# Kernel tuning notes

Measured on AMD Instinct MI355X. Metric: run time of the kernel, lower is better.

## Reference

```python
import jax, jax.numpy as jnp
import numpy as np

B, P, C = 64, 8732, 81
NEG_POS_RATIO = 3


def _smooth_l1_masked_sum(p, t, maskf):
    # smooth_l1 with beta=1, sum reduction, restricted to positive priors
    d = jnp.abs(p - t)
    l = jnp.where(d < 1.0, 0.5 * d * d, d - 0.5)  # [B,P,K]
    return jnp.sum(l.sum(-1) * maskf)


def setup_inputs() -> dict:
    key = jax.random.key(0)
    ks = jax.random.split(key, 6)
    loc_data = jax.random.normal(ks[0], (B, P, 4), jnp.float32)
    conf_data = jax.random.normal(ks[1], (B, P, C), jnp.float32)
    four_corners_data = jax.random.normal(ks[2], (B, P, 8), jnp.float32)
    loc_t = jax.random.normal(ks[3], (B, P, 4), jnp.float32)
    four_corners_t = jax.random.normal(ks[4], (B, P, 8), jnp.float32)
    conf_t = jax.random.randint(ks[5], (B, P), 0, C, jnp.int32)
    return {
        "loc_data": loc_data,
        "conf_data": conf_data,
        "four_corners_data": four_corners_data,
        "loc_t": loc_t,
        "four_corners_t": four_corners_t,
        "conf_t": conf_t,
    }


def reference(loc_data, conf_data, four_corners_data, loc_t, four_corners_t, conf_t):
    num_priors = conf_data.shape[1]
    pos = conf_t > 0                                  # [B,P]
    posf = pos.astype(conf_data.dtype)

    # localization + four-corner smooth-L1 over matched (positive) priors
    loss_l = _smooth_l1_masked_sum(loc_data, loc_t, posf)
    loss_four_corners = _smooth_l1_masked_sum(four_corners_data, four_corners_t, posf)

    # per-prior CE loss: log_sum_exp(conf) - conf[target]
    lse = jax.nn.logsumexp(conf_data, axis=-1)        # [B,P]
    gathered = jnp.take_along_axis(conf_data, conf_t[..., None], axis=-1)[..., 0]
    ce_all = lse - gathered                           # [B,P]

    # hard-negative mining: rank negatives by CE loss (double argsort)
    loss_c_mine = jnp.where(pos, 0.0, ce_all)
    loss_idx = jnp.argsort(-loss_c_mine, axis=1)      # descending sort indices
    idx_rank = jnp.argsort(loss_idx, axis=1)          # rank of each prior
    num_pos = pos.sum(axis=1, keepdims=True)          # [B,1]
    num_neg = jnp.minimum(NEG_POS_RATIO * num_pos, num_priors - 1)
    neg = idx_rank < num_neg                          # [B,P]

    sel = pos | neg
    loss_c = jnp.sum(jnp.where(sel, ce_all, 0.0))

    N = num_pos.sum().astype(conf_data.dtype)
    return (loss_l / N, loss_c / N, loss_four_corners / N)
```

## Files before the change

kernel.cpp:

```cpp
#include <hip/hip_runtime.h>


#define NB 64
#define NP 8732
#define NC 81
constexpr int BP = NB * NP;
constexpr int PBLK = (NP + 255) / 256;

__device__ inline float sl1(float d) {
    d = fabsf(d);
    return d < 1.0f ? 0.5f * d * d : d - 0.5f;
}

__global__ void k_init(float* acc_area) {
    if (threadIdx.x < 194) acc_area[threadIdx.x] = 0.0f;
}

__global__ __launch_bounds__(256) void k_main(
    const float* __restrict__ loc_data, const float* __restrict__ conf_data,
    const float* __restrict__ fc_data,  const float* __restrict__ loc_t,
    const float* __restrict__ fc_t,     const int* __restrict__ conf_t,
    float* __restrict__ ce, float* __restrict__ acc,
    int* __restrict__ npos_b, float* __restrict__ spos_b, float* __restrict__ sneg_b)
{
    const int b  = blockIdx.y;
    const int t  = threadIdx.x;
    const int p0 = blockIdx.x << 8;
    const int nrows = min(256, NP - p0);

    __shared__ __align__(16) float tile[64 * NC + 4];
    __shared__ int   tgt_s[256];
    __shared__ float red[4][5];

    float l_sum = 0.0f, f_sum = 0.0f, sp = 0.0f, sn = 0.0f;
    int np = 0;

    {
        const int p = p0 + t;
        int tgt = 0;
        if (p < NP) {
            const size_t g = (size_t)b * NP + p;
            tgt = conf_t[g];
            const float posf = (tgt > 0) ? 1.0f : 0.0f;
            np = (tgt > 0) ? 1 : 0;
            float4 a4  = ((const float4*)loc_data)[g];
            float4 a4t = ((const float4*)loc_t)[g];
            l_sum = (sl1(a4.x - a4t.x) + sl1(a4.y - a4t.y) +
                     sl1(a4.z - a4t.z) + sl1(a4.w - a4t.w)) * posf;
            float4 c0 = ((const float4*)fc_data)[2 * g];
            float4 c1 = ((const float4*)fc_data)[2 * g + 1];
            float4 d0 = ((const float4*)fc_t)[2 * g];
            float4 d1 = ((const float4*)fc_t)[2 * g + 1];
            f_sum = (sl1(c0.x - d0.x) + sl1(c0.y - d0.y) + sl1(c0.z - d0.z) + sl1(c0.w - d0.w) +
                     sl1(c1.x - d1.x) + sl1(c1.y - d1.y) + sl1(c1.z - d1.z) + sl1(c1.w - d1.w)) * posf;
        }
        tgt_s[t] = tgt;
    }

    const size_t gbase = ((size_t)b * NP + p0) * (size_t)NC;
    const int al = (int)(gbase & 3);
    const float* conf_al = conf_data + (gbase - (size_t)al);
    const int r = t >> 2, sub = t & 3;

    for (int s = 0; s < 4; ++s) {
        const int r0 = s << 6;
        const int rs = min(64, nrows - r0);
        if (rs <= 0) break;
        const int nf  = al + rs * NC;
        const int n4  = nf >> 2;
        const int rem = nf & 3;

        __syncthreads();
        const float4* src4 = (const float4*)(conf_al + (size_t)r0 * NC);
        float4* dst4 = (float4*)tile;
        for (int j = t; j < n4; j += 256) dst4[j] = src4[j];
        if (t < rem) tile[(n4 << 2) + t] = conf_al[(size_t)r0 * NC + (n4 << 2) + t];
        __syncthreads();

        if (r < rs) {
            const float* lrow = tile + al + r * NC;
            float s0 = 0.0f, s1 = 0.0f;
            int c = sub;
            #pragma unroll
            for (int k = 0; k < 10; ++k) {
                s0 += __expf(lrow[c]); c += 4;
                s1 += __expf(lrow[c]); c += 4;
            }
            if (sub == 0) s0 += __expf(lrow[80]);
            float ss = s0 + s1;
            ss += __shfl_xor(ss, 1, 64);
            ss += __shfl_xor(ss, 2, 64);
            if (sub == 0) {
                const int tgt = tgt_s[r0 + r];
                const float cev = __logf(ss) - lrow[tgt];
                ce[(size_t)b * NP + (size_t)(p0 + r0 + r)] = cev;
                if (tgt > 0) sp += cev; else sn += cev;
            }
        }
    }

    const int wave = t >> 6, lane = t & 63;
    float vnp = (float)np;
    #pragma unroll
    for (int o = 32; o; o >>= 1) {
        l_sum += __shfl_xor(l_sum, o, 64);
        f_sum += __shfl_xor(f_sum, o, 64);
        sp    += __shfl_xor(sp, o, 64);
        sn    += __shfl_xor(sn, o, 64);
        vnp   += __shfl_xor(vnp, o, 64);
    }
    if (lane == 0) {
        red[wave][0] = l_sum; red[wave][1] = f_sum;
        red[wave][2] = sp;    red[wave][3] = sn;   red[wave][4] = vnp;
    }
    __syncthreads();
    if (t == 0) {
        float rl = 0, rf = 0, rp = 0, rn = 0, rc = 0;
        #pragma unroll
        for (int w = 0; w < 4; ++w) {
            rl += red[w][0]; rf += red[w][1]; rp += red[w][2];
            rn += red[w][3]; rc += red[w][4];
        }
        atomicAdd(&acc[0], rl);
        atomicAdd(&acc[1], rf);
        atomicAdd(&spos_b[b], rp);
        atomicAdd(&sneg_b[b], rn);
        atomicAdd(&npos_b[b], (int)rc);
    }
}

__global__ __launch_bounds__(256) void k_batch(
    const float* __restrict__ ce, const int* __restrict__ conf_t,
    const int* __restrict__ npos_b, const float* __restrict__ spos_b,
    const float* __restrict__ sneg_b, float* __restrict__ loss_c_b)
{
    const int b = blockIdx.x;
    const int t = threadIdx.x;
    const int npos    = npos_b[b];
    const int nneg    = NP - npos;
    const int num_neg = min(3 * npos, NP - 1);

    if (num_neg >= nneg) {
        if (t == 0) loss_c_b[b] = spos_b[b] + sneg_b[b];
        return;
    }
    if (num_neg <= 0) {
        if (t == 0) loss_c_b[b] = spos_b[b];
        return;
    }

    __shared__ float ce_s[NP];
    __shared__ float sredf[4];
    __shared__ int   sredi[4];
    const float* crow = ce + (size_t)b * NP;
    const int*   trow = conf_t + (size_t)b * NP;
    for (int p = t; p < NP; p += 256)
        ce_s[p] = (trow[p] > 0) ? -1.0f : crow[p];
    __syncthreads();

    const int wave = t >> 6, lane = t & 63;
    const int K = num_neg;
    unsigned lo = 0u, hi = 0x7f800000u;
    while (lo < hi) {
        unsigned mid = lo + ((hi - lo) >> 1);
        float v = __uint_as_float(mid);
        int c_t = 0;
        for (int p = t; p < NP; p += 256) c_t += (ce_s[p] > v) ? 1 : 0;
        #pragma unroll
        for (int o = 32; o; o >>= 1) c_t += __shfl_xor(c_t, o, 64);
        __syncthreads();
        if (lane == 0) sredi[wave] = c_t;
        __syncthreads();
        int cnt = sredi[0] + sredi[1] + sredi[2] + sredi[3];
        if (cnt < K) hi = mid; else lo = mid + 1;
    }
    float v = __uint_as_float(lo);
    int c_t = 0; float s_t = 0.0f;
    for (int p = t; p < NP; p += 256) {
        float x = ce_s[p];
        if (x > v) { c_t++; s_t += x; }
    }
    #pragma unroll
    for (int o = 32; o; o >>= 1) {
        c_t += __shfl_xor(c_t, o, 64);
        s_t += __shfl_xor(s_t, o, 64);
    }
    __syncthreads();
    if (lane == 0) { sredi[wave] = c_t; sredf[wave] = s_t; }
    __syncthreads();
    if (t == 0) {
        int   cnt = sredi[0] + sredi[1] + sredi[2] + sredi[3];
        float sgt = sredf[0] + sredf[1] + sredf[2] + sredf[3];
        loss_c_b[b] = spos_b[b] + sgt + (float)(K - cnt) * v;
    }
}

__global__ void k_final(const float* __restrict__ acc,
                        const float* __restrict__ loss_c_b,
                        const int* __restrict__ npos_b,
                        float* __restrict__ out)
{
    const int t = threadIdx.x;
    float lc = loss_c_b[t];
    int   np = npos_b[t];
    #pragma unroll
    for (int o = 32; o; o >>= 1) {
        lc += __shfl_xor(lc, o, 64);
        np += __shfl_xor(np, o, 64);
    }
    if (t == 0) {
        float N = (float)np;
        out[0] = acc[0] / N;
        out[1] = lc / N;
        out[2] = acc[1] / N;
    }
}

extern "C" void kernel_launch(void* const* d_in, const int* in_sizes, int n_in,
                              void* d_out, int out_size, void* d_ws, size_t ws_size,
                              hipStream_t stream)
{
    const float* loc_data  = (const float*)d_in[0];
    const float* conf_data = (const float*)d_in[1];
    const float* fc_data   = (const float*)d_in[2];
    const float* loc_t     = (const float*)d_in[3];
    const float* fc_t      = (const float*)d_in[4];
    const int*   conf_t    = (const int*)d_in[5];
    float* out = (float*)d_out;

    float* ce       = (float*)d_ws;
    float* acc      = ce + BP;
    int*   npos_b   = (int*)(acc + 2);
    float* spos_b   = (float*)(npos_b + 64);
    float* sneg_b   = spos_b + 64;
    float* loss_c_b = sneg_b + 64;

    hipLaunchKernelGGL(k_init,  dim3(1), dim3(256), 0, stream, acc);
    hipLaunchKernelGGL(k_main,  dim3(PBLK, NB), dim3(256), 0, stream,
                       loc_data, conf_data, fc_data, loc_t, fc_t, conf_t,
                       ce, acc, npos_b, spos_b, sneg_b);
    hipLaunchKernelGGL(k_batch, dim3(NB), dim3(256), 0, stream,
                       ce, conf_t, npos_b, spos_b, sneg_b, loss_c_b);
    hipLaunchKernelGGL(k_final, dim3(1), dim3(64), 0, stream,
                       acc, loss_c_b, npos_b, out);
}
```

Before: 339.0 us.

## Double-buffer conf tiles with direct global-to-LDS loads in k_main

Replaces the synchronous float4 copy of 64-row conf tiles into shared memory with `global_load_lds` (16-byte) loads into two 32-row buffers. The next phase is prefetched while the current one is reduced, with manual `s_waitcnt` and barriers. Each row now uses 8 lanes instead of 4, with an extra shuffle step in the reduction. The goal is to overlap conf_data memory latency with the exp/log compute. The trade-offs are hand-written wait counts, extra barriers, and fixed 256-float chunk loads that can read slightly past the end of the final tile.

```diff
diff --git a/kernel.cpp b/kernel.cpp
--- a/kernel.cpp
+++ b/kernel.cpp
@@ -6,10 +6,19 @@
 #define NC 81
 constexpr int BP = NB * NP;
 constexpr int PBLK = (NP + 255) / 256;
+constexpr int PROWS = 32;
+constexpr int TFLOAT = 11 * 256;
 
 __device__ inline float sl1(float d) {
     d = fabsf(d);
     return d < 1.0f ? 0.5f * d * d : d - 0.5f;
+}
+
+__device__ __forceinline__ void gload_lds16(const float* g, float* l) {
+    __builtin_amdgcn_global_load_lds(
+        (const __attribute__((address_space(1))) void*)g,
+        (__attribute__((address_space(3))) void*)l,
+        16, 0, 0);
 }
 
 __global__ void k_init(float* acc_area) {
@@ -27,8 +36,9 @@
     const int t  = threadIdx.x;
     const int p0 = blockIdx.x << 8;
     const int nrows = min(256, NP - p0);
-
-    __shared__ __align__(16) float tile[64 * NC + 4];
+    const int nph   = (nrows + PROWS - 1) / PROWS;
+
+    __shared__ __align__(16) float tile[2][TFLOAT];
     __shared__ int   tgt_s[256];
     __shared__ float red[4][5];
 
@@ -60,46 +70,57 @@
     const size_t gbase = ((size_t)b * NP + p0) * (size_t)NC;
     const int al = (int)(gbase & 3);
     const float* conf_al = conf_data + (gbase - (size_t)al);
-    const int r = t >> 2, sub = t & 3;
-
-    for (int s = 0; s < 4; ++s) {
-        const int r0 = s << 6;
-        const int rs = min(64, nrows - r0);
-        if (rs <= 0) break;
-        const int nf  = al + rs * NC;
-        const int n4  = nf >> 2;
-        const int rem = nf & 3;
-
-        __syncthreads();
-        const float4* src4 = (const float4*)(conf_al + (size_t)r0 * NC);
-        float4* dst4 = (float4*)tile;
-        for (int j = t; j < n4; j += 256) dst4[j] = src4[j];
-        if (t < rem) tile[(n4 << 2) + t] = conf_al[(size_t)r0 * NC + (n4 << 2) + t];
-        __syncthreads();
-
+    const int wave = t >> 6, lane = t & 63;
+    const int r = t >> 3, sub = t & 7;
+
+    auto stage = [&](int s) {
+        const int rs  = min(PROWS, nrows - s * PROWS);
+        const int nch = (al + rs * NC + 255) >> 8;
+        const float* gb = conf_al + (size_t)s * (PROWS * NC);
+        float* lb = tile[s & 1];
+        #pragma unroll
+        for (int i = 0; i < 3; ++i) {
+            int c = wave + 4 * i;
+            c = c < nch ? c : nch - 1;
+            gload_lds16(gb + ((size_t)c << 8) + (lane << 2), lb + (c << 8));
+        }
+    };
+
+    stage(0);
+    for (int s = 0; s < nph; ++s) {
+        if (s + 1 < nph) {
+            stage(s + 1);
+            asm volatile("s_waitcnt vmcnt(3)\n\ts_barrier" ::: "memory");
+        } else {
+            asm volatile("s_waitcnt vmcnt(0)\n\ts_barrier" ::: "memory");
+        }
+
+        const int rs = min(PROWS, nrows - s * PROWS);
         if (r < rs) {
-            const float* lrow = tile + al + r * NC;
+            const float* lrow = tile[s & 1] + al + r * NC;
             float s0 = 0.0f, s1 = 0.0f;
             int c = sub;
             #pragma unroll
-            for (int k = 0; k < 10; ++k) {
-                s0 += __expf(lrow[c]); c += 4;
-                s1 += __expf(lrow[c]); c += 4;
+            for (int k = 0; k < 5; ++k) {
+                s0 += __expf(lrow[c]); c += 8;
+                s1 += __expf(lrow[c]); c += 8;
             }
             if (sub == 0) s0 += __expf(lrow[80]);
             float ss = s0 + s1;
             ss += __shfl_xor(ss, 1, 64);
             ss += __shfl_xor(ss, 2, 64);
+            ss += __shfl_xor(ss, 4, 64);
             if (sub == 0) {
-                const int tgt = tgt_s[r0 + r];
+                const int pl = s * PROWS + r;
+                const int tgt = tgt_s[pl];
                 const float cev = __logf(ss) - lrow[tgt];
-                ce[(size_t)b * NP + (size_t)(p0 + r0 + r)] = cev;
+                ce[(size_t)b * NP + (size_t)(p0 + pl)] = cev;
                 if (tgt > 0) sp += cev; else sn += cev;
             }
         }
-    }
-
-    const int wave = t >> 6, lane = t & 63;
+        asm volatile("s_barrier" ::: "memory");
+    }
+
     float vnp = (float)np;
     #pragma unroll
     for (int o = 32; o; o >>= 1) {
```

After: 321.8 us. -5.0%, faster.

## Compute per-row CE with wave-wide direct global loads instead of LDS tiling

Applied to the files above, without the earlier changes.

Drops the shared-memory staging of the 64x81 confidence tile. Each wave now processes its 64 rows one at a time, with every lane loading one or two logits directly from global memory and prefetching the next row. The sum of exponentials is reduced with cross-lane shuffles and the target logit is picked with a shuffle. This removes LDS traffic and block barriers, but the 64 rows are handled serially with a full 6-step shuffle reduction per row, and each row is fetched with small partially-coalesced loads, which lowers per-thread parallelism.

```diff
diff --git a/kernel.cpp b/kernel.cpp
--- a/kernel.cpp
+++ b/kernel.cpp
@@ -26,9 +26,7 @@
     const int b  = blockIdx.y;
     const int t  = threadIdx.x;
     const int p0 = blockIdx.x << 8;
-    const int nrows = min(256, NP - p0);
-
-    __shared__ __align__(16) float tile[64 * NC + 4];
+
     __shared__ int   tgt_s[256];
     __shared__ float red[4][5];
 
@@ -56,50 +54,43 @@
         }
         tgt_s[t] = tgt;
     }
-
-    const size_t gbase = ((size_t)b * NP + p0) * (size_t)NC;
-    const int al = (int)(gbase & 3);
-    const float* conf_al = conf_data + (gbase - (size_t)al);
-    const int r = t >> 2, sub = t & 3;
-
-    for (int s = 0; s < 4; ++s) {
-        const int r0 = s << 6;
-        const int rs = min(64, nrows - r0);
-        if (rs <= 0) break;
-        const int nf  = al + rs * NC;
-        const int n4  = nf >> 2;
-        const int rem = nf & 3;
-
-        __syncthreads();
-        const float4* src4 = (const float4*)(conf_al + (size_t)r0 * NC);
-        float4* dst4 = (float4*)tile;
-        for (int j = t; j < n4; j += 256) dst4[j] = src4[j];
-        if (t < rem) tile[(n4 << 2) + t] = conf_al[(size_t)r0 * NC + (n4 << 2) + t];
-        __syncthreads();
-
-        if (r < rs) {
-            const float* lrow = tile + al + r * NC;
-            float s0 = 0.0f, s1 = 0.0f;
-            int c = sub;
+    __syncthreads();
+
+    const int wave = t >> 6, lane = t & 63;
+    const int rbase = p0 + (wave << 6);
+    const int rs = min(64, max(0, NP - rbase));
+    float v_ce = 0.0f;
+
+    if (rs > 0) {
+        const float* rowp = conf_data + ((size_t)b * NP + rbase) * (size_t)NC;
+        float a0 = rowp[lane];
+        float a1 = rowp[17 + lane];
+        int   tg = tgt_s[wave << 6];
+
+        for (int i = 0; i < rs; ++i) {
+            float b0 = 0.0f, b1 = 0.0f; int tgn = 0;
+            if (i + 1 < rs) {
+                const float* nxt = rowp + NC;
+                b0  = nxt[lane];
+                b1  = nxt[17 + lane];
+                tgn = tgt_s[(wave << 6) + i + 1];
+            }
+            float e = __expf(a0) + ((lane >= 47) ? __expf(a1) : 0.0f);
             #pragma unroll
-            for (int k = 0; k < 10; ++k) {
-                s0 += __expf(lrow[c]); c += 4;
-                s1 += __expf(lrow[c]); c += 4;
+            for (int o = 32; o; o >>= 1) e += __shfl_xor(e, o, 64);
+            float tv = (tg < 64) ? __shfl(a0, tg, 64)
+                                 : __shfl(a1, tg - 17, 64);
+            float cev = __logf(e) - tv;
+            if (lane == i) {
+                v_ce = cev;
+                if (tg > 0) sp += cev; else sn += cev;
             }
-            if (sub == 0) s0 += __expf(lrow[80]);
-            float ss = s0 + s1;
-            ss += __shfl_xor(ss, 1, 64);
-            ss += __shfl_xor(ss, 2, 64);
-            if (sub == 0) {
-                const int tgt = tgt_s[r0 + r];
-                const float cev = __logf(ss) - lrow[tgt];
-                ce[(size_t)b * NP + (size_t)(p0 + r0 + r)] = cev;
-                if (tgt > 0) sp += cev; else sn += cev;
-            }
+            a0 = b0; a1 = b1; tg = tgn; rowp += NC;
         }
-    }
-
-    const int wave = t >> 6, lane = t & 63;
+        if (lane < rs)
+            ce[(size_t)b * NP + (size_t)(rbase + lane)] = v_ce;
+    }
+
     float vnp = (float)np;
     #pragma unroll
     for (int o = 32; o; o >>= 1) {
```

Measured after the change: 394.2 us. 16.3% more time.
